# Kernel tuning notes

Measured on AMD Instinct MI355X. Metric: run time of the kernel, lower is better.

## Reference

```python
import jax, jax.numpy as jnp
import numpy as np

D_MODEL = 512
D_STATE = 64
N_LAYERS = 6
L_SEQ = 784
BATCH = 64


def _layernorm(x, g, b, eps=1e-5):
    mu = x.mean(-1, keepdims=True)
    var = ((x - mu) ** 2).mean(-1, keepdims=True)
    return (x - mu) * jax.lax.rsqrt(var + eps) * g + b


def _s4d_kernel(log_dt, log_A_real, A_imag, C_re, C_im, L):
    # log_dt: (H,), others: (H, N). Returns real conv kernel (H, L).
    dt = jnp.exp(log_dt)[:, None]                      # (H,1)
    A = -jnp.exp(log_A_real) + 1j * A_imag             # (H,N) complex
    C = C_re + 1j * C_im                               # (H,N)
    dtA = A * dt                                       # (H,N)
    Cd = C * (jnp.exp(dtA) - 1.0) / A                  # ZOH-discretized C
    # Vandermonde: V[h,n,l] = exp(dtA[h,n] * l)
    V = jnp.exp(dtA[:, :, None] * jnp.arange(L, dtype=jnp.float32))  # (H,N,L)
    K = 2.0 * jnp.einsum('hn,hnl->hl', Cd, V).real     # (H,L)
    return K


def _s4_fftconv(u, K, D):
    # u: (B,L,H), K: (H,L), D: (H,)
    L = u.shape[1]
    uf = jnp.fft.rfft(u, 2 * L, axis=1)                # (B, L+1, H)
    kf = jnp.fft.rfft(K.T, 2 * L, axis=0)              # (L+1, H)
    y = jnp.fft.irfft(uf * kf[None], 2 * L, axis=1)[:, :L]
    return y + u * D


def setup_inputs() -> dict:
    key = jax.random.key(0)
    ks = jax.random.split(key, 12)
    H, N, NL = D_MODEL, D_STATE, N_LAYERS
    x = jax.random.normal(ks[0], (BATCH, L_SEQ, 1), dtype=jnp.float32)
    enc_w = jax.random.normal(ks[1], (1, H), dtype=jnp.float32) * 0.5
    enc_b = jnp.zeros((H,), dtype=jnp.float32)
    # S4D-Lin style init, stacked over layers
    log_dt = jnp.tile(
        jax.random.uniform(ks[2], (H,), minval=np.log(0.001), maxval=np.log(0.1)),
        (NL, 1))                                        # (NL,H)
    log_A_real = jnp.full((NL, H, N), jnp.log(0.5), dtype=jnp.float32)
    A_imag = jnp.tile(np.pi * jnp.arange(N, dtype=jnp.float32), (NL, H, 1))
    C_re = jax.random.normal(ks[3], (NL, H, N), dtype=jnp.float32) * (0.5 ** 0.5)
    C_im = jax.random.normal(ks[4], (NL, H, N), dtype=jnp.float32) * (0.5 ** 0.5)
    D = jax.random.normal(ks[5], (NL, H), dtype=jnp.float32)
    ln_g = jnp.ones((NL, H), dtype=jnp.float32)
    ln_b = jnp.zeros((NL, H), dtype=jnp.float32)
    fn_g = jnp.ones((H,), dtype=jnp.float32)
    fn_b = jnp.zeros((H,), dtype=jnp.float32)
    dec_w = jax.random.normal(ks[6], (H, 10), dtype=jnp.float32) / jnp.sqrt(H)
    dec_b = jnp.zeros((10,), dtype=jnp.float32)
    return dict(x=x, enc_w=enc_w, enc_b=enc_b, log_dt=log_dt,
                log_A_real=log_A_real, A_imag=A_imag, C_re=C_re, C_im=C_im,
                D=D, ln_g=ln_g, ln_b=ln_b, fn_g=fn_g, fn_b=fn_b,
                dec_w=dec_w, dec_b=dec_b)


def reference(x, enc_w, enc_b, log_dt, log_A_real, A_imag, C_re, C_im, D,
              ln_g, ln_b, fn_g, fn_b, dec_w, dec_b):
    h = x @ enc_w + enc_b                               # (B,L,H)
    L = h.shape[1]
    for i in range(log_dt.shape[0]):                    # fixed n_layers
        K = _s4d_kernel(log_dt[i], log_A_real[i], A_imag[i], C_re[i], C_im[i], L)
        z = _s4_fftconv(h, K, D[i])                     # S4 output (dropout=eval)
        h = _layernorm(h + z, ln_g[i], ln_b[i])         # residual + LN
    h = _layernorm(h, fn_g, fn_b)
    h = h.mean(axis=1)                                  # mean pool over seq
    return h @ dec_w + dec_b                            # (B,10)
```

## Files before the change

### kernel.cpp

```cpp
#include <hip/hip_runtime.h>
#include <hip/hip_bf16.h>

#define HD 512
#define NST 64
#define NLAY 6
#define LSEQ 784
#define BB 64
#define NKA 848
#define TOFF 800
#define LPADROWS 800
#define KSTR 850
#define CHK2 5
#define NCH 5
#define UTS2 9

typedef unsigned short u16;
typedef short s8v __attribute__((ext_vector_type(8)));
typedef float f16v __attribute__((ext_vector_type(16)));
typedef u16  u4h __attribute__((ext_vector_type(4)));
typedef u16  u8h __attribute__((ext_vector_type(8)));

__device__ __forceinline__ unsigned f2b(float f)
{
    unsigned u = __builtin_bit_cast(unsigned, f);
    return (u + 0x7FFFu + ((u >> 16) & 1u)) >> 16;
}
__device__ __forceinline__ float b2f16(u16 v)
{
    unsigned u = ((unsigned)v) << 16;
    return __builtin_bit_cast(float, u);
}
__device__ __forceinline__ unsigned pkbf(float lo, float hi)
{
    unsigned r;
    asm("v_cvt_pk_bf16_f32 %0, %1, %2" : "=v"(r) : "v"(lo), "v"(hi));
    return r;
}

__global__ void precompute_k(const float* __restrict__ log_dt,
                             const float* __restrict__ log_A_real,
                             const float* __restrict__ A_imag,
                             const float* __restrict__ C_re,
                             const float* __restrict__ C_im,
                             float* __restrict__ lamr, float* __restrict__ lami,
                             float* __restrict__ dtr,  float* __restrict__ dti,
                             float* __restrict__ c2r,  float* __restrict__ c2i)
{
    int t = blockIdx.x * 256 + threadIdx.x;
    if (t >= NLAY * HD * NST) return;
    int ih = t >> 6;
    float dt  = expf(log_dt[ih]);
    float are = -expf(log_A_real[t]);
    float aim = A_imag[t];
    float dr = are * dt, di = aim * dt;
    float er = expf(dr);
    float sn, cs; __sincosf(di, &sn, &cs);
    float lr = er * cs, li = er * sn;
    float e1r = lr - 1.0f, e1i = li;
    float den = are * are + aim * aim;
    float qr = (e1r * are + e1i * aim) / den;
    float qi = (e1i * are - e1r * aim) / den;
    float crv = C_re[t], civ = C_im[t];
    lamr[t] = lr; lami[t] = li; dtr[t] = dr; dti[t] = di;
    c2r[t] = 2.0f * (crv * qr - civ * qi);
    c2i[t] = 2.0f * (crv * qi + civ * qr);
}

__global__ void kq_k(const float* __restrict__ lamr, const float* __restrict__ lami,
                     const float* __restrict__ dtr,  const float* __restrict__ dti,
                     const float* __restrict__ c2r,  const float* __restrict__ c2i,
                     u16* __restrict__ KA)
{
    int t = blockIdx.x * 256 + threadIdx.x;
    int dc = t % 49;
    int ih = t / 49;
    int d0 = dc * 16;
    float acc[16];
#pragma unroll
    for (int k = 0; k < 16; k++) acc[k] = 0.f;
    int base = ih * 64;
    for (int n = 0; n < 64; n++) {
        float lr = lamr[base + n], li = lami[base + n];
        float dr = dtr[base + n],  di = dti[base + n];
        float cr = c2r[base + n],  ci = c2i[base + n];
        float e = __expf(dr * (float)d0);
        float sn, cs; __sincosf(di * (float)d0, &sn, &cs);
        float pr = e * cs, pi = e * sn;
#pragma unroll
        for (int k = 0; k < 16; k++) {
            acc[k] = fmaf(cr, pr, fmaf(-ci, pi, acc[k]));
            float nr = pr * lr - pi * li;
            pi = fmaf(pr, li, pi * lr);
            pr = nr;
        }
    }
    u16* kap = KA + (size_t)ih * NKA;
#pragma unroll
    for (int k = 0; k < 16; k++)
        kap[TOFF - (d0 + k)] = (u16)f2b(acc[k]);
    if (dc == 0)  for (int z = TOFF + 1; z < NKA; z++) kap[z] = 0;
    if (dc == 48) for (int z = 0; z < TOFF - 783; z++) kap[z] = 0;
}

__global__ void xt_k(const float* __restrict__ x, float* __restrict__ xT)
{
    int t = blockIdx.x * 256 + threadIdx.x;
    int l = t >> 6, b = t & 63;
    xT[t] = x[b * LSEQ + l];
}

__global__ void encoder_k(const float* __restrict__ xT, const float* __restrict__ ew,
                          const float* __restrict__ eb, u16* __restrict__ Vb)
{
    int g = blockIdx.x * 256 + threadIdx.x;
    int bo = g & 7;
    int h  = (g >> 3) & 511;
    int l  = g >> 12;
    const float4* xp = (const float4*)&xT[l * BB + 8 * bo];
    float4 a0 = xp[0], a1 = xp[1];
    float w = ew[h], bb = eb[h];
    unsigned p0 = f2b(fmaf(a0.x, w, bb)) | (f2b(fmaf(a0.y, w, bb)) << 16);
    unsigned p1 = f2b(fmaf(a0.z, w, bb)) | (f2b(fmaf(a0.w, w, bb)) << 16);
    unsigned p2 = f2b(fmaf(a1.x, w, bb)) | (f2b(fmaf(a1.y, w, bb)) << 16);
    unsigned p3 = f2b(fmaf(a1.z, w, bb)) | (f2b(fmaf(a1.w, w, bb)) << 16);
    *(uint4*)&Vb[((size_t)l * HD + h) * BB + 8 * bo] = (uint4){p0, p1, p2, p3};
}

__global__ __launch_bounds__(256)
void stats_k(const u16* __restrict__ P, float2* __restrict__ M)
{
    __shared__ float redS[32][65], redQ[32][65];
    const int thr = threadIdx.x;
    const size_t l = blockIdx.x;
    if (l >= LSEQ) {
        if (thr < BB) M[l * BB + thr] = make_float2(0.f, 1.f);
        return;
    }
    const int bo = thr & 7;
    const int ho = thr >> 3;
    const u16* sp = &P[(l * HD + (size_t)ho * 16) * BB + 8 * bo];
    float s[8] = {0, 0, 0, 0, 0, 0, 0, 0};
    float q[8] = {0, 0, 0, 0, 0, 0, 0, 0};
#pragma unroll
    for (int k = 0; k < 16; k++) {
        u8h r = *(const u8h*)(sp + (size_t)k * BB);
#pragma unroll
        for (int i = 0; i < 8; i++) {
            float x = b2f16(r[i]);
            s[i] += x;
            q[i] = fmaf(x, x, q[i]);
        }
    }
#pragma unroll
    for (int i = 0; i < 8; i++) { redS[ho][8 * bo + i] = s[i]; redQ[ho][8 * bo + i] = q[i]; }
    __syncthreads();
    if (thr < 64) {
        float ts = 0.f, tq = 0.f;
#pragma unroll
        for (int g = 0; g < 32; g++) { ts += redS[g][thr]; tq += redQ[g][thr]; }
        float mu = ts * (1.0f / HD);
        float rs = rsqrtf(tq * (1.0f / HD) - mu * mu + 1e-5f);
        M[l * BB + thr] = make_float2(mu, rs);
    }
}

template<int FLN>
__global__ __launch_bounds__(128, 4)
void conv_k(const u16* __restrict__ Vb, u16* __restrict__ V2,
            const u16* __restrict__ KA, const float* __restrict__ Dvec,
            const float2* __restrict__ M,
            const float* __restrict__ gp, const float* __restrict__ bp)
{
    __shared__ __align__(16) u16 KR[6816];
    __shared__ __align__(16) unsigned UT[2][64 * UTS2];

    const int thr = threadIdx.x;
    const int bid = blockIdx.x;
    const int c   = NCH - 1 - (bid >> 9);
    const int h   = bid & 511;
    const int w   = thr >> 6;
    const int lane = thr & 63;
    const int n2 = lane & 31;
    const int qp = lane >> 5;
    const int JTN = 10 * c + 10;

    const float gh = FLN ? gp[h] : 0.f;
    const float bh = FLN ? bp[h] : 0.f;

    const u16* kap = KA + (size_t)h * NKA;
    {
        int s = thr & 7, ch = thr >> 3;
        int i0 = ch * 53;
        int i1 = (i0 + 53 < NKA) ? (i0 + 53) : NKA;
        u16* kr = KR + KSTR * s + ((8 - s) & 7);
        for (int i = i0; i < i1; i++) kr[i] = kap[i];
    }

    const int jj = thr >> 4;
    const int bq = thr & 15;
    {
        const int j = 2 * jj;
        const u16* p = &Vb[((size_t)j * HD + h) * BB + 4 * bq];
        u4h r0 = *(const u4h*)p;
        u4h r1 = *(const u4h*)(p + (size_t)HD * BB);
        unsigned* up = &UT[0][0];
        if (FLN) {
            const float4* m0p = (const float4*)&M[(size_t)j * BB + 4 * bq];
            const float4* m1p = (const float4*)&M[(size_t)(j + 1) * BB + 4 * bq];
            float4 a0 = m0p[0], a1 = m0p[1], b0 = m1p[0], b1 = m1p[1];
            float A0[4] = {a0.y * gh, a0.w * gh, a1.y * gh, a1.w * gh};
            float C0[4] = {fmaf(-a0.x, A0[0], bh), fmaf(-a0.z, A0[1], bh),
                           fmaf(-a1.x, A0[2], bh), fmaf(-a1.z, A0[3], bh)};
            float A1[4] = {b0.y * gh, b0.w * gh, b1.y * gh, b1.w * gh};
            float C1[4] = {fmaf(-b0.x, A1[0], bh), fmaf(-b0.z, A1[1], bh),
                           fmaf(-b1.x, A1[2], bh), fmaf(-b1.z, A1[3], bh)};
#pragma unroll
            for (int i = 0; i < 4; i++) {
                float x0 = fmaf(b2f16(r0[i]), A0[i], C0[i]);
                float x1 = fmaf(b2f16(r1[i]), A1[i], C1[i]);
                up[(4 * bq + i) * UTS2 + jj] = pkbf(x0, x1);
            }
        } else {
#pragma unroll
            for (int i = 0; i < 4; i++)
                up[(4 * bq + i) * UTS2 + jj] = (unsigned)r0[i] | ((unsigned)r1[i] << 16);
        }
    }
    __syncthreads();

    f16v acc[CHK2];
#pragma unroll
    for (int i = 0; i < CHK2; i++)
#pragma unroll
        for (int r = 0; r < 16; r++) acc[i][r] = 0.f;

    const float dcoef = 1.0f + Dvec[h];

    const int s = lane & 7;
    const u16* krb = KR + KSTR * s + ((8 - s) & 7)
                     + (TOFF - 160 * c) + 8 * qp - n2;
    const unsigned* bb0 = &UT[0][(32 * w + n2) * UTS2 + 4 * qp];
    const unsigned* bb1 = &UT[1][(32 * w + n2) * UTS2 + 4 * qp];

    for (int jt = 0; jt < JTN; ++jt) {
        u4h r0, r1;
        float4 mA0, mB0, mA1, mB1;
        const bool more = (jt + 1) < JTN;
        if (more) {
            int j = 16 * (jt + 1) + 2 * jj;
            const u16* p = &Vb[((size_t)j * HD + h) * BB + 4 * bq];
            r0 = *(const u4h*)p;
            r1 = *(const u4h*)(p + (size_t)HD * BB);
            if (FLN) {
                const float4* m0p = (const float4*)&M[(size_t)j * BB + 4 * bq];
                const float4* m1p = (const float4*)&M[(size_t)(j + 1) * BB + 4 * bq];
                mA0 = m0p[0]; mB0 = m0p[1]; mA1 = m1p[0]; mB1 = m1p[1];
            }
        }
        const unsigned* bb = (jt & 1) ? bb1 : bb0;
        union { unsigned u[4]; s8v v; } bu;
        bu.u[0] = bb[0]; bu.u[1] = bb[1]; bu.u[2] = bb[2]; bu.u[3] = bb[3];

        const u16* ap0 = krb + 16 * jt;
#pragma unroll
        for (int lt = 0; lt < CHK2; ++lt) {
            if (jt > 10 * c + 2 * lt + 1) continue;
            s8v av = *(const s8v*)__builtin_assume_aligned(ap0 - 32 * lt, 16);
            acc[lt] = __builtin_amdgcn_mfma_f32_32x32x16_bf16(av, bu.v, acc[lt], 0, 0, 0);
        }
        if (more) {
            unsigned* up = &UT[(jt & 1) ^ 1][0];
            if (FLN) {
                float A0[4] = {mA0.y * gh, mA0.w * gh, mB0.y * gh, mB0.w * gh};
                float C0[4] = {fmaf(-mA0.x, A0[0], bh), fmaf(-mA0.z, A0[1], bh),
                               fmaf(-mB0.x, A0[2], bh), fmaf(-mB0.z, A0[3], bh)};
                float A1[4] = {mA1.y * gh, mA1.w * gh, mB1.y * gh, mB1.w * gh};
                float C1[4] = {fmaf(-mA1.x, A1[0], bh), fmaf(-mA1.z, A1[1], bh),
                               fmaf(-mB1.x, A1[2], bh), fmaf(-mB1.z, A1[3], bh)};
#pragma unroll
                for (int i = 0; i < 4; i++) {
                    float x0 = fmaf(b2f16(r0[i]), A0[i], C0[i]);
                    float x1 = fmaf(b2f16(r1[i]), A1[i], C1[i]);
                    up[(4 * bq + i) * UTS2 + jj] = pkbf(x0, x1);
                }
            } else {
#pragma unroll
                for (int i = 0; i < 4; i++)
                    up[(4 * bq + i) * UTS2 + jj] = (unsigned)r0[i] | ((unsigned)r1[i] << 16);
            }
        }
        __syncthreads();
    }

#pragma unroll
    for (int lt = 0; lt < CHK2; ++lt) {
        const int l0 = 32 * (5 * c + lt) + 4 * qp;
#pragma unroll
        for (int r = 0; r < 16; ++r) {
            int l = l0 + (r & 3) + 8 * (r >> 2);
            size_t a = ((size_t)l * HD + h) * BB + 32 * w + n2;
            float x = b2f16(Vb[a]);
            float u = x;
            if (FLN) {
                float2 m = M[(size_t)l * BB + 32 * w + n2];
                u = fmaf(x - m.x, m.y * gh, bh);
            }
            V2[a] = (u16)f2b(fmaf(dcoef, u, acc[lt][r]));
        }
    }
}

__global__ __launch_bounds__(512)
void lnT2_k(const u16* __restrict__ src, u16* __restrict__ dst,
            const float2* __restrict__ M,
            const float* __restrict__ g5p, const float* __restrict__ b5p,
            const float* __restrict__ gp, const float* __restrict__ bp)
{
    __shared__ float redS[64][65], redQ[64][65];
    __shared__ float mus[64], rss[64];
    __shared__ float gs[512], bs[512];
    const int thr = threadIdx.x;
    const int bo = thr & 7;
    const int hg = thr >> 3;
    const size_t l = blockIdx.x;
    gs[thr] = gp[thr]; bs[thr] = bp[thr];

    const float4* mp = (const float4*)&M[l * BB + 8 * bo];
    float4 m0 = mp[0], m1 = mp[1], m2 = mp[2], m3 = mp[3];
    float mu5[8] = {m0.x, m0.z, m1.x, m1.z, m2.x, m2.z, m3.x, m3.z};
    float rs5[8] = {m0.y, m0.w, m1.y, m1.w, m2.y, m2.w, m3.y, m3.w};

    const u16* sp = &src[(l * HD + (size_t)hg * 8) * BB + 8 * bo];
    float v[64];
    float s[8] = {0, 0, 0, 0, 0, 0, 0, 0};
    float q[8] = {0, 0, 0, 0, 0, 0, 0, 0};
#pragma unroll
    for (int k = 0; k < 8; k++) {
        u8h r = *(const u8h*)(sp + (size_t)k * BB);
        float g5 = g5p[hg * 8 + k], b5 = b5p[hg * 8 + k];
#pragma unroll
        for (int i = 0; i < 8; i++) {
            float x = fmaf(b2f16(r[i]) - mu5[i], rs5[i] * g5, b5);
            v[k * 8 + i] = x;
            s[i] += x;
            q[i] = fmaf(x, x, q[i]);
        }
    }
#pragma unroll
    for (int i = 0; i < 8; i++) { redS[hg][8 * bo + i] = s[i]; redQ[hg][8 * bo + i] = q[i]; }
    __syncthreads();
    if (thr < 64) {
        float ts = 0.f, tq = 0.f;
#pragma unroll
        for (int g = 0; g < 64; g++) { ts += redS[g][thr]; tq += redQ[g][thr]; }
        float mu = ts * (1.0f / HD);
        mus[thr] = mu;
        rss[thr] = rsqrtf(tq * (1.0f / HD) - mu * mu + 1e-5f);
    }
    __syncthreads();
    float mu[8], rs[8];
#pragma unroll
    for (int i = 0; i < 8; i++) { mu[i] = mus[8 * bo + i]; rs[i] = rss[8 * bo + i]; }
    u16* dp = &dst[(l * HD + (size_t)hg * 8) * BB + 8 * bo];
#pragma unroll
    for (int k = 0; k < 8; k++) {
        float g = gs[hg * 8 + k], bb = bs[hg * 8 + k];
        u8h wv;
#pragma unroll
        for (int i = 0; i < 8; i++)
            wv[i] = (u16)f2b(fmaf((v[k * 8 + i] - mu[i]) * rs[i], g, bb));
        *(u8h*)(dp + (size_t)k * BB) = wv;
    }
}

__global__ void pool_k(const u16* __restrict__ Vb, float* __restrict__ PO)
{
    __shared__ float red[4][64];
    int h = blockIdx.x;
    int b = threadIdx.x & 63;
    int lg = threadIdx.x >> 6;
    const u16* p = &Vb[(size_t)h * BB + b];
    float s = 0.f;
    for (int l = lg; l < LSEQ; l += 4) s += b2f16(p[(size_t)l * HD * BB]);
    red[lg][b] = s;
    __syncthreads();
    if (threadIdx.x < 64) {
        float t = red[0][b] + red[1][b] + red[2][b] + red[3][b];
        PO[h * BB + b] = t * (1.0f / LSEQ);
    }
}

__global__ void dec_k(const float* __restrict__ PO, const float* __restrict__ w,
                      const float* __restrict__ bias, float* __restrict__ out)
{
    int t = blockIdx.x * 256 + threadIdx.x;
    if (t >= BB * 10) return;
    int cc = t % 10, b = t / 10;
    float acc = bias[cc];
    for (int hh = 0; hh < HD; hh++)
        acc = fmaf(PO[hh * BB + b], w[hh * 10 + cc], acc);
    out[t] = acc;
}

extern "C" void kernel_launch(void* const* d_in, const int* in_sizes, int n_in,
                              void* d_out, int out_size, void* d_ws, size_t ws_size,
                              hipStream_t stream)
{
    const float* x   = (const float*)d_in[0];
    const float* ew  = (const float*)d_in[1];
    const float* eb  = (const float*)d_in[2];
    const float* ldt = (const float*)d_in[3];
    const float* lar = (const float*)d_in[4];
    const float* aim = (const float*)d_in[5];
    const float* cre = (const float*)d_in[6];
    const float* cim = (const float*)d_in[7];
    const float* Dp  = (const float*)d_in[8];
    const float* lng = (const float*)d_in[9];
    const float* lnb = (const float*)d_in[10];
    const float* fng = (const float*)d_in[11];
    const float* fnb = (const float*)d_in[12];
    const float* dw  = (const float*)d_in[13];
    const float* db  = (const float*)d_in[14];
    float* out = (float*)d_out;

    const size_t SZB = (size_t)BB * LPADROWS * HD;
    const size_t PP  = (size_t)NLAY * HD * NST;
    u16*   Vb  = (u16*)d_ws;
    u16*   V2  = Vb + SZB;
    float* PAR = (float*)(V2 + SZB);
    float* lamr = PAR,        * lami = PAR + PP;
    float* dtr  = PAR + 2*PP, * dti  = PAR + 3*PP;
    float* c2r  = PAR + 4*PP, * c2i  = PAR + 5*PP;
    u16* KA = (u16*)(PAR + 6 * PP);
    float* PO = PAR + 6 * PP + (NLAY * HD * NKA) / 2;
    float* xT = PO + BB * HD;
    float2* M = (float2*)PAR;

    precompute_k<<<(NLAY * HD * NST + 255) / 256, 256, 0, stream>>>(
        ldt, lar, aim, cre, cim, lamr, lami, dtr, dti, c2r, c2i);
    kq_k<<<(NLAY * HD * 49) / 256, 256, 0, stream>>>(
        lamr, lami, dtr, dti, c2r, c2i, KA);
    xt_k<<<(LSEQ * BB) / 256, 256, 0, stream>>>(x, xT);
    encoder_k<<<(LSEQ * HD * 8) / 256, 256, 0, stream>>>(xT, ew, eb, Vb);

    conv_k<0><<<512 * NCH, 128, 0, stream>>>(Vb, V2, KA, Dp, M, lng, lnb);
    stats_k<<<LPADROWS, 256, 0, stream>>>(V2, M);
    for (int i = 1; i < NLAY; i++) {
        const u16* srcb = (i & 1) ? V2 : Vb;
        u16*       dstb = (i & 1) ? Vb : V2;
        conv_k<1><<<512 * NCH, 128, 0, stream>>>(
            srcb, dstb, KA + (size_t)i * HD * NKA, Dp + i * HD,
            M, lng + (size_t)(i - 1) * HD, lnb + (size_t)(i - 1) * HD);
        stats_k<<<LPADROWS, 256, 0, stream>>>(dstb, M);
    }
    lnT2_k<<<LSEQ, 512, 0, stream>>>(Vb, Vb, M, lng + 5 * HD, lnb + 5 * HD, fng, fnb);
    pool_k<<<HD, 256, 0, stream>>>(Vb, PO);
    dec_k<<<(BB * 10 + 255) / 256, 256, 0, stream>>>(PO, dw, db, out);
}
```

Before: 656.5 us.

## Restructure causal conv to keep Toeplitz kernel fragments in registers per channel

Replaces the chunked conv kernel (512x5 blocks, kernel row staged in LDS) with one block per channel. Each block preloads all 25x2 Toeplitz A-fragments into registers from a dual-shifted kernel layout, so every fragment load is aligned. The block then stages the whole padded input sequence into a large swizzled LDS buffer in five groups and reuses it for the residual/D term in the epilogue. The intent is to drop the per-chunk kernel reloads and the redundant input re-reads across chunks. In exchange it launches only 512 blocks with heavy register pressure (launch_bounds 128,1) and large LDS, which hurts occupancy and latency hiding.

```diff
diff --git a/kernel.cpp b/kernel.cpp
--- a/kernel.cpp
+++ b/kernel.cpp
@@ -6,18 +6,13 @@
 #define NLAY 6
 #define LSEQ 784
 #define BB 64
-#define NKA 848
 #define TOFF 800
 #define LPADROWS 800
-#define KSTR 850
-#define CHK2 5
-#define NCH 5
-#define UTS2 9
+#define KROW 850
 
 typedef unsigned short u16;
 typedef short s8v __attribute__((ext_vector_type(8)));
 typedef float f16v __attribute__((ext_vector_type(16)));
-typedef u16  u4h __attribute__((ext_vector_type(4)));
 typedef u16  u8h __attribute__((ext_vector_type(8)));
 
 __device__ __forceinline__ unsigned f2b(float f)
@@ -69,7 +64,7 @@
 __global__ void kq_k(const float* __restrict__ lamr, const float* __restrict__ lami,
                      const float* __restrict__ dtr,  const float* __restrict__ dti,
                      const float* __restrict__ c2r,  const float* __restrict__ c2i,
-                     u16* __restrict__ KA)
+                     u16* __restrict__ KAS)
 {
     int t = blockIdx.x * 256 + threadIdx.x;
     int dc = t % 49;
@@ -94,12 +89,23 @@
             pr = nr;
         }
     }
-    u16* kap = KA + (size_t)ih * NKA;
-#pragma unroll
-    for (int k = 0; k < 16; k++)
-        kap[TOFF - (d0 + k)] = (u16)f2b(acc[k]);
-    if (dc == 0)  for (int z = TOFF + 1; z < NKA; z++) kap[z] = 0;
-    if (dc == 48) for (int z = 0; z < TOFF - 783; z++) kap[z] = 0;
+    u16* r0p = KAS + (size_t)ih * 2 * KROW;
+    u16* r1p = r0p + KROW;
+#pragma unroll
+    for (int k = 0; k < 16; k++) {
+        u16 vb = (u16)f2b(acc[k]);
+        int tt = TOFF - (d0 + k);
+        r0p[tt] = vb;
+        r1p[1 + tt] = vb;
+    }
+    if (dc == 0) {
+        for (int z = TOFF + 1; z < KROW; z++) r0p[z] = 0;
+        for (int z = TOFF + 2; z < KROW; z++) r1p[z] = 0;
+        r1p[0] = 0;
+    }
+    if (dc == 48) {
+        for (int z = 0; z < TOFF - 783; z++) { r0p[z] = 0; r1p[1 + z] = 0; }
+    }
 }
 
 __global__ void xt_k(const float* __restrict__ x, float* __restrict__ xT)
@@ -116,6 +122,8 @@
     int bo = g & 7;
     int h  = (g >> 3) & 511;
     int l  = g >> 12;
+    uint4* dst = (uint4*)&Vb[((size_t)l * HD + h) * BB + 8 * bo];
+    if (l >= LSEQ) { *dst = (uint4){0, 0, 0, 0}; return; }
     const float4* xp = (const float4*)&xT[l * BB + 8 * bo];
     float4 a0 = xp[0], a1 = xp[1];
     float w = ew[h], bb = eb[h];
@@ -123,7 +131,7 @@
     unsigned p1 = f2b(fmaf(a0.z, w, bb)) | (f2b(fmaf(a0.w, w, bb)) << 16);
     unsigned p2 = f2b(fmaf(a1.x, w, bb)) | (f2b(fmaf(a1.y, w, bb)) << 16);
     unsigned p3 = f2b(fmaf(a1.z, w, bb)) | (f2b(fmaf(a1.w, w, bb)) << 16);
-    *(uint4*)&Vb[((size_t)l * HD + h) * BB + 8 * bo] = (uint4){p0, p1, p2, p3};
+    *dst = (uint4){p0, p1, p2, p3};
 }
 
 __global__ __launch_bounds__(256)
@@ -165,148 +173,140 @@
 }
 
 template<int FLN>
-__global__ __launch_bounds__(128, 4)
-void conv_k(const u16* __restrict__ Vb, u16* __restrict__ V2,
-            const u16* __restrict__ KA, const float* __restrict__ Dvec,
-            const float2* __restrict__ M,
-            const float* __restrict__ gp, const float* __restrict__ bp)
-{
-    __shared__ __align__(16) u16 KR[6816];
-    __shared__ __align__(16) unsigned UT[2][64 * UTS2];
+__global__ __launch_bounds__(128, 1)
+void sconv_k(const u16* __restrict__ Vb, u16* __restrict__ V2,
+             const u16* __restrict__ KAS, const float* __restrict__ Dvec,
+             const float2* __restrict__ M,
+             const float* __restrict__ gp, const float* __restrict__ bp)
+{
+    __shared__ __align__(16) unsigned SB[25 * 64 * 20];
 
     const int thr = threadIdx.x;
-    const int bid = blockIdx.x;
-    const int c   = NCH - 1 - (bid >> 9);
-    const int h   = bid & 511;
+    const int h   = blockIdx.x;
+    const int lane = thr & 63;
     const int w   = thr >> 6;
-    const int lane = thr & 63;
-    const int n2 = lane & 31;
-    const int qp = lane >> 5;
-    const int JTN = 10 * c + 10;
+    const int n2  = lane & 31;
+    const int qp  = lane >> 5;
 
     const float gh = FLN ? gp[h] : 0.f;
     const float bh = FLN ? bp[h] : 0.f;
-
-    const u16* kap = KA + (size_t)h * NKA;
+    const float dcoef = 1.0f + Dvec[h];
+
+    s8v afr[25][2];
     {
-        int s = thr & 7, ch = thr >> 3;
-        int i0 = ch * 53;
-        int i1 = (i0 + 53 < NKA) ? (i0 + 53) : NKA;
-        u16* kr = KR + KSTR * s + ((8 - s) & 7);
-        for (int i = i0; i < i1; i++) kr[i] = kap[i];
-    }
-
-    const int jj = thr >> 4;
-    const int bq = thr & 15;
-    {
-        const int j = 2 * jj;
-        const u16* p = &Vb[((size_t)j * HD + h) * BB + 4 * bq];
-        u4h r0 = *(const u4h*)p;
-        u4h r1 = *(const u4h*)(p + (size_t)HD * BB);
-        unsigned* up = &UT[0][0];
-        if (FLN) {
-            const float4* m0p = (const float4*)&M[(size_t)j * BB + 4 * bq];
-            const float4* m1p = (const float4*)&M[(size_t)(j + 1) * BB + 4 * bq];
-            float4 a0 = m0p[0], a1 = m0p[1], b0 = m1p[0], b1 = m1p[1];
-            float A0[4] = {a0.y * gh, a0.w * gh, a1.y * gh, a1.w * gh};
-            float C0[4] = {fmaf(-a0.x, A0[0], bh), fmaf(-a0.z, A0[1], bh),
-                           fmaf(-a1.x, A0[2], bh), fmaf(-a1.z, A0[3], bh)};
-            float A1[4] = {b0.y * gh, b0.w * gh, b1.y * gh, b1.w * gh};
-            float C1[4] = {fmaf(-b0.x, A1[0], bh), fmaf(-b0.z, A1[1], bh),
-                           fmaf(-b1.x, A1[2], bh), fmaf(-b1.z, A1[3], bh)};
-#pragma unroll
-            for (int i = 0; i < 4; i++) {
-                float x0 = fmaf(b2f16(r0[i]), A0[i], C0[i]);
-                float x1 = fmaf(b2f16(r1[i]), A1[i], C1[i]);
-                up[(4 * bq + i) * UTS2 + jj] = pkbf(x0, x1);
+        const int sA = n2 & 1;
+        const u16* kb = KAS + ((size_t)h * 2 + sA) * KROW + sA
+                        + TOFF - n2 + 8 * qp;
+#pragma unroll
+        for (int dd = 0; dd < 25; dd++)
+#pragma unroll
+            for (int ch = 0; ch < 2; ch++) {
+                const u16* kp = kb - 32 * dd + 16 * ch;
+                union { unsigned uu[4]; s8v v; } af;
+#pragma unroll
+                for (int q = 0; q < 4; q++)
+                    af.uu[q] = *(const unsigned*)(kp + 2 * q);
+                afr[dd][ch] = af.v;
             }
-        } else {
-#pragma unroll
-            for (int i = 0; i < 4; i++)
-                up[(4 * bq + i) * UTS2 + jj] = (unsigned)r0[i] | ((unsigned)r1[i] << 16);
-        }
-    }
-    __syncthreads();
-
-    f16v acc[CHK2];
-#pragma unroll
-    for (int i = 0; i < CHK2; i++)
-#pragma unroll
-        for (int r = 0; r < 16; r++) acc[i][r] = 0.f;
-
-    const float dcoef = 1.0f + Dvec[h];
-
-    const int s = lane & 7;
-    const u16* krb = KR + KSTR * s + ((8 - s) & 7)
-                     + (TOFF - 160 * c) + 8 * qp - n2;
-    const unsigned* bb0 = &UT[0][(32 * w + n2) * UTS2 + 4 * qp];
-    const unsigned* bb1 = &UT[1][(32 * w + n2) * UTS2 + 4 * qp];
-
-    for (int jt = 0; jt < JTN; ++jt) {
-        u4h r0, r1;
-        float4 mA0, mB0, mA1, mB1;
-        const bool more = (jt + 1) < JTN;
-        if (more) {
-            int j = 16 * (jt + 1) + 2 * jj;
-            const u16* p = &Vb[((size_t)j * HD + h) * BB + 4 * bq];
-            r0 = *(const u4h*)p;
-            r1 = *(const u4h*)(p + (size_t)HD * BB);
+    }
+
+    auto STAGE = [&](int g0) {
+#pragma unroll
+        for (int j5 = 0; j5 < 5; j5++) {
+            int u  = thr + 128 * j5;
+            int rp = u >> 3;
+            int sg = u & 7;
+            int r0 = 160 * g0 + 2 * rp;
+            const u16* p = &Vb[((size_t)r0 * HD + h) * BB + 8 * sg];
+            u8h ra = *(const u8h*)p;
+            u8h rb = *(const u8h*)(p + (size_t)HD * BB);
+            unsigned ov[8];
             if (FLN) {
-                const float4* m0p = (const float4*)&M[(size_t)j * BB + 4 * bq];
-                const float4* m1p = (const float4*)&M[(size_t)(j + 1) * BB + 4 * bq];
-                mA0 = m0p[0]; mB0 = m0p[1]; mA1 = m1p[0]; mB1 = m1p[1];
-            }
-        }
-        const unsigned* bb = (jt & 1) ? bb1 : bb0;
-        union { unsigned u[4]; s8v v; } bu;
-        bu.u[0] = bb[0]; bu.u[1] = bb[1]; bu.u[2] = bb[2]; bu.u[3] = bb[3];
-
-        const u16* ap0 = krb + 16 * jt;
-#pragma unroll
-        for (int lt = 0; lt < CHK2; ++lt) {
-            if (jt > 10 * c + 2 * lt + 1) continue;
-            s8v av = *(const s8v*)__builtin_assume_aligned(ap0 - 32 * lt, 16);
-            acc[lt] = __builtin_amdgcn_mfma_f32_32x32x16_bf16(av, bu.v, acc[lt], 0, 0, 0);
-        }
-        if (more) {
-            unsigned* up = &UT[(jt & 1) ^ 1][0];
-            if (FLN) {
-                float A0[4] = {mA0.y * gh, mA0.w * gh, mB0.y * gh, mB0.w * gh};
-                float C0[4] = {fmaf(-mA0.x, A0[0], bh), fmaf(-mA0.z, A0[1], bh),
-                               fmaf(-mB0.x, A0[2], bh), fmaf(-mB0.z, A0[3], bh)};
-                float A1[4] = {mA1.y * gh, mA1.w * gh, mB1.y * gh, mB1.w * gh};
-                float C1[4] = {fmaf(-mA1.x, A1[0], bh), fmaf(-mA1.z, A1[1], bh),
-                               fmaf(-mB1.x, A1[2], bh), fmaf(-mB1.z, A1[3], bh)};
+                const float4* m0 = (const float4*)&M[(size_t)r0 * BB + 8 * sg];
+                const float4* m1 = (const float4*)&M[(size_t)(r0 + 1) * BB + 8 * sg];
 #pragma unroll
                 for (int i = 0; i < 4; i++) {
-                    float x0 = fmaf(b2f16(r0[i]), A0[i], C0[i]);
-                    float x1 = fmaf(b2f16(r1[i]), A1[i], C1[i]);
-                    up[(4 * bq + i) * UTS2 + jj] = pkbf(x0, x1);
+                    float4 ma = m0[i], mb = m1[i];
+                    float A0 = ma.y * gh, C0 = fmaf(-ma.x, A0, bh);
+                    float A1 = ma.w * gh, C1 = fmaf(-ma.z, A1, bh);
+                    float B0 = mb.y * gh, D0 = fmaf(-mb.x, B0, bh);
+                    float B1 = mb.w * gh, D1 = fmaf(-mb.z, B1, bh);
+                    float x0 = fmaf(b2f16(ra[2 * i]),     A0, C0);
+                    float x1 = fmaf(b2f16(ra[2 * i + 1]), A1, C1);
+                    float y0 = fmaf(b2f16(rb[2 * i]),     B0, D0);
+                    float y1 = fmaf(b2f16(rb[2 * i + 1]), B1, D1);
+                    ov[2 * i]     = pkbf(x0, y0);
+                    ov[2 * i + 1] = pkbf(x1, y1);
                 }
             } else {
 #pragma unroll
-                for (int i = 0; i < 4; i++)
-                    up[(4 * bq + i) * UTS2 + jj] = (unsigned)r0[i] | ((unsigned)r1[i] << 16);
+                for (int i = 0; i < 8; i++)
+                    ov[i] = (unsigned)ra[i] | ((unsigned)rb[i] << 16);
             }
-        }
+            int tt = 5 * g0 + (rp >> 4);
+            int jj = rp & 15;
+            unsigned* dst = &SB[(tt * 64 + 8 * sg) * 20 + (jj ^ ((sg & 3) << 2))];
+#pragma unroll
+            for (int k = 0; k < 8; k++) dst[k * 20] = ov[k];
+        }
+    };
+
+    const int bcol = 32 * w + n2;
+    const int swz  = ((bcol >> 3) & 3) << 2;
+    const unsigned* bb0 = &SB[bcol * 20 + ((4 * qp) ^ swz)];
+    const unsigned* bb1 = &SB[bcol * 20 + ((8 + 4 * qp) ^ swz)];
+
+    STAGE(0);
+    __syncthreads();
+
+#pragma unroll
+    for (int g = 0; g < 5; g++) {
+        f16v acc[5];
+#pragma unroll
+        for (int i = 0; i < 5; i++)
+#pragma unroll
+            for (int r = 0; r < 16; r++) acc[i][r] = 0.f;
+
+#pragma unroll
+        for (int t = 0; t < 25; t++) {
+            if (t <= 5 * g + 4) {
+                s8v bv0 = *(const s8v*)__builtin_assume_aligned(bb0 + t * 1280, 16);
+                s8v bv1 = *(const s8v*)__builtin_assume_aligned(bb1 + t * 1280, 16);
+#pragma unroll
+                for (int Ti = 0; Ti < 5; Ti++) {
+                    if (5 * g + Ti >= t) {
+                        acc[Ti] = __builtin_amdgcn_mfma_f32_32x32x16_bf16(
+                            afr[5 * g + Ti - t][0], bv0, acc[Ti], 0, 0, 0);
+                        acc[Ti] = __builtin_amdgcn_mfma_f32_32x32x16_bf16(
+                            afr[5 * g + Ti - t][1], bv1, acc[Ti], 0, 0, 0);
+                    }
+                }
+            }
+        }
+
+#pragma unroll
+        for (int Ti = 0; Ti < 5; Ti++) {
+            const int T = 5 * g + Ti;
+#pragma unroll
+            for (int k = 0; k < 4; k++) {
+                int jjE = (2 * qp + 4 * k) ^ swz;
+                const uint2 dw = *(const uint2*)__builtin_assume_aligned(
+                    &SB[(T * 64 + bcol) * 20 + jjE], 8);
+                float u0 = b2f16((u16)(dw.x & 0xffff));
+                float u1 = b2f16((u16)(dw.x >> 16));
+                float u2 = b2f16((u16)(dw.y & 0xffff));
+                float u3 = b2f16((u16)(dw.y >> 16));
+                int l = 32 * T + 8 * k + 4 * qp;
+                size_t a = ((size_t)l * HD + h) * BB + bcol;
+                V2[a]                       = (u16)f2b(fmaf(dcoef, u0, acc[Ti][4 * k + 0]));
+                V2[a + (size_t)HD * BB]     = (u16)f2b(fmaf(dcoef, u1, acc[Ti][4 * k + 1]));
+                V2[a + (size_t)2 * HD * BB] = (u16)f2b(fmaf(dcoef, u2, acc[Ti][4 * k + 2]));
+                V2[a + (size_t)3 * HD * BB] = (u16)f2b(fmaf(dcoef, u3, acc[Ti][4 * k + 3]));
+            }
+        }
+
+        if (g < 4) STAGE(g + 1);
         __syncthreads();
-    }
-
-#pragma unroll
-    for (int lt = 0; lt < CHK2; ++lt) {
-        const int l0 = 32 * (5 * c + lt) + 4 * qp;
-#pragma unroll
-        for (int r = 0; r < 16; ++r) {
-            int l = l0 + (r & 3) + 8 * (r >> 2);
-            size_t a = ((size_t)l * HD + h) * BB + 32 * w + n2;
-            float x = b2f16(Vb[a]);
-            float u = x;
-            if (FLN) {
-                float2 m = M[(size_t)l * BB + 32 * w + n2];
-                u = fmaf(x - m.x, m.y * gh, bh);
-            }
-            V2[a] = (u16)f2b(fmaf(dcoef, u, acc[lt][r]));
-        }
     }
 }
 
@@ -431,25 +431,25 @@
     float* lamr = PAR,        * lami = PAR + PP;
     float* dtr  = PAR + 2*PP, * dti  = PAR + 3*PP;
     float* c2r  = PAR + 4*PP, * c2i  = PAR + 5*PP;
-    u16* KA = (u16*)(PAR + 6 * PP);
-    float* PO = PAR + 6 * PP + (NLAY * HD * NKA) / 2;
+    u16* KAS = (u16*)(PAR + 6 * PP);
+    float* PO = (float*)(KAS + (size_t)NLAY * HD * 2 * KROW);
     float* xT = PO + BB * HD;
     float2* M = (float2*)PAR;
 
     precompute_k<<<(NLAY * HD * NST + 255) / 256, 256, 0, stream>>>(
         ldt, lar, aim, cre, cim, lamr, lami, dtr, dti, c2r, c2i);
     kq_k<<<(NLAY * HD * 49) / 256, 256, 0, stream>>>(
-        lamr, lami, dtr, dti, c2r, c2i, KA);
+        lamr, lami, dtr, dti, c2r, c2i, KAS);
     xt_k<<<(LSEQ * BB) / 256, 256, 0, stream>>>(x, xT);
-    encoder_k<<<(LSEQ * HD * 8) / 256, 256, 0, stream>>>(xT, ew, eb, Vb);
-
-    conv_k<0><<<512 * NCH, 128, 0, stream>>>(Vb, V2, KA, Dp, M, lng, lnb);
+    encoder_k<<<(LPADROWS * HD * 8) / 256, 256, 0, stream>>>(xT, ew, eb, Vb);
+
+    sconv_k<0><<<HD, 128, 0, stream>>>(Vb, V2, KAS, Dp, M, lng, lnb);
     stats_k<<<LPADROWS, 256, 0, stream>>>(V2, M);
     for (int i = 1; i < NLAY; i++) {
         const u16* srcb = (i & 1) ? V2 : Vb;
         u16*       dstb = (i & 1) ? Vb : V2;
-        conv_k<1><<<512 * NCH, 128, 0, stream>>>(
-            srcb, dstb, KA + (size_t)i * HD * NKA, Dp + i * HD,
+        sconv_k<1><<<HD, 128, 0, stream>>>(
+            srcb, dstb, KAS + (size_t)i * HD * 2 * KROW, Dp + i * HD,
             M, lng + (size_t)(i - 1) * HD, lnb + (size_t)(i - 1) * HD);
         stats_k<<<LPADROWS, 256, 0, stream>>>(dstb, M);
     }
```

Result: slower. 860.9 us (+31.1%).

## Prefetch conv input two tiles ahead and interleave kernel-gen state updates

Applied to the files above, without the earlier changes.

The conv kernel's global-to-LDS staging becomes a two-deep software pipeline. Loads for tile jt+2 are issued before the MFMAs of tile jt, and the LDS write for tile jt+1 happens between the B-fragment read and the MFMAs, which gives global latency more time to hide. The Vandermonde kernel-generation loop now processes four states at once, exposing independent FMA chains for more ILP. The encoder also zero-fills the padded rows up to LPADROWS, because the deeper prefetch now reads those rows and must see defined data.

```diff
diff --git a/kernel.cpp b/kernel.cpp
--- a/kernel.cpp
+++ b/kernel.cpp
@@ -79,19 +79,27 @@
 #pragma unroll
     for (int k = 0; k < 16; k++) acc[k] = 0.f;
     int base = ih * 64;
-    for (int n = 0; n < 64; n++) {
-        float lr = lamr[base + n], li = lami[base + n];
-        float dr = dtr[base + n],  di = dti[base + n];
-        float cr = c2r[base + n],  ci = c2i[base + n];
-        float e = __expf(dr * (float)d0);
-        float sn, cs; __sincosf(di * (float)d0, &sn, &cs);
-        float pr = e * cs, pi = e * sn;
+    for (int n = 0; n < 64; n += 4) {
+        float lr[4], li[4], cr[4], ci[4], pr[4], pi[4];
+#pragma unroll
+        for (int j = 0; j < 4; j++) {
+            int q = base + n + j;
+            lr[j] = lamr[q]; li[j] = lami[q];
+            float dr = dtr[q], di = dti[q];
+            cr[j] = c2r[q]; ci[j] = c2i[q];
+            float e = __expf(dr * (float)d0);
+            float sn, cs; __sincosf(di * (float)d0, &sn, &cs);
+            pr[j] = e * cs; pi[j] = e * sn;
+        }
 #pragma unroll
         for (int k = 0; k < 16; k++) {
-            acc[k] = fmaf(cr, pr, fmaf(-ci, pi, acc[k]));
-            float nr = pr * lr - pi * li;
-            pi = fmaf(pr, li, pi * lr);
-            pr = nr;
+#pragma unroll
+            for (int j = 0; j < 4; j++) {
+                acc[k] = fmaf(cr[j], pr[j], fmaf(-ci[j], pi[j], acc[k]));
+                float nr = pr[j] * lr[j] - pi[j] * li[j];
+                pi[j] = fmaf(pr[j], li[j], pi[j] * lr[j]);
+                pr[j] = nr;
+            }
         }
     }
     u16* kap = KA + (size_t)ih * NKA;
@@ -116,6 +124,8 @@
     int bo = g & 7;
     int h  = (g >> 3) & 511;
     int l  = g >> 12;
+    uint4* dst = (uint4*)&Vb[((size_t)l * HD + h) * BB + 8 * bo];
+    if (l >= LSEQ) { *dst = (uint4){0, 0, 0, 0}; return; }
     const float4* xp = (const float4*)&xT[l * BB + 8 * bo];
     float4 a0 = xp[0], a1 = xp[1];
     float w = ew[h], bb = eb[h];
@@ -123,7 +133,7 @@
     unsigned p1 = f2b(fmaf(a0.z, w, bb)) | (f2b(fmaf(a0.w, w, bb)) << 16);
     unsigned p2 = f2b(fmaf(a1.x, w, bb)) | (f2b(fmaf(a1.y, w, bb)) << 16);
     unsigned p3 = f2b(fmaf(a1.z, w, bb)) | (f2b(fmaf(a1.w, w, bb)) << 16);
-    *(uint4*)&Vb[((size_t)l * HD + h) * BB + 8 * bo] = (uint4){p0, p1, p2, p3};
+    *dst = (uint4){p0, p1, p2, p3};
 }
 
 __global__ __launch_bounds__(256)
@@ -198,22 +208,29 @@
 
     const int jj = thr >> 4;
     const int bq = thr & 15;
-    {
-        const int j = 2 * jj;
+
+    auto LOADT = [&](int jt, u4h& r0, u4h& r1,
+                     float4& mA0, float4& mB0, float4& mA1, float4& mB1) {
+        int j = 16 * jt + 2 * jj;
         const u16* p = &Vb[((size_t)j * HD + h) * BB + 4 * bq];
-        u4h r0 = *(const u4h*)p;
-        u4h r1 = *(const u4h*)(p + (size_t)HD * BB);
-        unsigned* up = &UT[0][0];
+        r0 = *(const u4h*)p;
+        r1 = *(const u4h*)(p + (size_t)HD * BB);
         if (FLN) {
             const float4* m0p = (const float4*)&M[(size_t)j * BB + 4 * bq];
             const float4* m1p = (const float4*)&M[(size_t)(j + 1) * BB + 4 * bq];
-            float4 a0 = m0p[0], a1 = m0p[1], b0 = m1p[0], b1 = m1p[1];
-            float A0[4] = {a0.y * gh, a0.w * gh, a1.y * gh, a1.w * gh};
-            float C0[4] = {fmaf(-a0.x, A0[0], bh), fmaf(-a0.z, A0[1], bh),
-                           fmaf(-a1.x, A0[2], bh), fmaf(-a1.z, A0[3], bh)};
-            float A1[4] = {b0.y * gh, b0.w * gh, b1.y * gh, b1.w * gh};
-            float C1[4] = {fmaf(-b0.x, A1[0], bh), fmaf(-b0.z, A1[1], bh),
-                           fmaf(-b1.x, A1[2], bh), fmaf(-b1.z, A1[3], bh)};
+            mA0 = m0p[0]; mB0 = m0p[1]; mA1 = m1p[0]; mB1 = m1p[1];
+        }
+    };
+    auto WRITET = [&](int jt, u4h r0, u4h r1,
+                      float4 mA0, float4 mB0, float4 mA1, float4 mB1) {
+        unsigned* up = &UT[jt & 1][0];
+        if (FLN) {
+            float A0[4] = {mA0.y * gh, mA0.w * gh, mB0.y * gh, mB0.w * gh};
+            float C0[4] = {fmaf(-mA0.x, A0[0], bh), fmaf(-mA0.z, A0[1], bh),
+                           fmaf(-mB0.x, A0[2], bh), fmaf(-mB0.z, A0[3], bh)};
+            float A1[4] = {mA1.y * gh, mA1.w * gh, mB1.y * gh, mB1.w * gh};
+            float C1[4] = {fmaf(-mA1.x, A1[0], bh), fmaf(-mA1.z, A1[1], bh),
+                           fmaf(-mB1.x, A1[2], bh), fmaf(-mB1.z, A1[3], bh)};
 #pragma unroll
             for (int i = 0; i < 4; i++) {
                 float x0 = fmaf(b2f16(r0[i]), A0[i], C0[i]);
@@ -225,7 +242,15 @@
             for (int i = 0; i < 4; i++)
                 up[(4 * bq + i) * UTS2 + jj] = (unsigned)r0[i] | ((unsigned)r1[i] << 16);
         }
-    }
+    };
+
+    {
+        u4h t0, t1; float4 a0, a1, a2, a3;
+        LOADT(0, t0, t1, a0, a1, a2, a3);
+        WRITET(0, t0, t1, a0, a1, a2, a3);
+    }
+    u4h cr0, cr1; float4 cm0, cm1, cm2, cm3;
+    LOADT(1, cr0, cr1, cm0, cm1, cm2, cm3);
     __syncthreads();
 
     f16v acc[CHK2];
@@ -242,24 +267,15 @@
     const unsigned* bb0 = &UT[0][(32 * w + n2) * UTS2 + 4 * qp];
     const unsigned* bb1 = &UT[1][(32 * w + n2) * UTS2 + 4 * qp];
 
+    u4h nr0, nr1; float4 nm0, nm1, nm2, nm3;
     for (int jt = 0; jt < JTN; ++jt) {
-        u4h r0, r1;
-        float4 mA0, mB0, mA1, mB1;
-        const bool more = (jt + 1) < JTN;
-        if (more) {
-            int j = 16 * (jt + 1) + 2 * jj;
-            const u16* p = &Vb[((size_t)j * HD + h) * BB + 4 * bq];
-            r0 = *(const u4h*)p;
-            r1 = *(const u4h*)(p + (size_t)HD * BB);
-            if (FLN) {
-                const float4* m0p = (const float4*)&M[(size_t)j * BB + 4 * bq];
-                const float4* m1p = (const float4*)&M[(size_t)(j + 1) * BB + 4 * bq];
-                mA0 = m0p[0]; mB0 = m0p[1]; mA1 = m1p[0]; mB1 = m1p[1];
-            }
-        }
+        if (jt + 2 < JTN) LOADT(jt + 2, nr0, nr1, nm0, nm1, nm2, nm3);
+
         const unsigned* bb = (jt & 1) ? bb1 : bb0;
         union { unsigned u[4]; s8v v; } bu;
         bu.u[0] = bb[0]; bu.u[1] = bb[1]; bu.u[2] = bb[2]; bu.u[3] = bb[3];
+
+        if (jt + 1 < JTN) WRITET(jt + 1, cr0, cr1, cm0, cm1, cm2, cm3);
 
         const u16* ap0 = krb + 16 * jt;
 #pragma unroll
@@ -268,27 +284,8 @@
             s8v av = *(const s8v*)__builtin_assume_aligned(ap0 - 32 * lt, 16);
             acc[lt] = __builtin_amdgcn_mfma_f32_32x32x16_bf16(av, bu.v, acc[lt], 0, 0, 0);
         }
-        if (more) {
-            unsigned* up = &UT[(jt & 1) ^ 1][0];
-            if (FLN) {
-                float A0[4] = {mA0.y * gh, mA0.w * gh, mB0.y * gh, mB0.w * gh};
-                float C0[4] = {fmaf(-mA0.x, A0[0], bh), fmaf(-mA0.z, A0[1], bh),
-                               fmaf(-mB0.x, A0[2], bh), fmaf(-mB0.z, A0[3], bh)};
-                float A1[4] = {mA1.y * gh, mA1.w * gh, mB1.y * gh, mB1.w * gh};
-                float C1[4] = {fmaf(-mA1.x, A1[0], bh), fmaf(-mA1.z, A1[1], bh),
-                               fmaf(-mB1.x, A1[2], bh), fmaf(-mB1.z, A1[3], bh)};
-#pragma unroll
-                for (int i = 0; i < 4; i++) {
-                    float x0 = fmaf(b2f16(r0[i]), A0[i], C0[i]);
-                    float x1 = fmaf(b2f16(r1[i]), A1[i], C1[i]);
-                    up[(4 * bq + i) * UTS2 + jj] = pkbf(x0, x1);
-                }
-            } else {
-#pragma unroll
-                for (int i = 0; i < 4; i++)
-                    up[(4 * bq + i) * UTS2 + jj] = (unsigned)r0[i] | ((unsigned)r1[i] << 16);
-            }
-        }
+        cr0 = nr0; cr1 = nr1;
+        cm0 = nm0; cm1 = nm1; cm2 = nm2; cm3 = nm3;
         __syncthreads();
     }
 
@@ -441,7 +438,7 @@
     kq_k<<<(NLAY * HD * 49) / 256, 256, 0, stream>>>(
         lamr, lami, dtr, dti, c2r, c2i, KA);
     xt_k<<<(LSEQ * BB) / 256, 256, 0, stream>>>(x, xT);
-    encoder_k<<<(LSEQ * HD * 8) / 256, 256, 0, stream>>>(xT, ew, eb, Vb);
+    encoder_k<<<(LPADROWS * HD * 8) / 256, 256, 0, stream>>>(xT, ew, eb, Vb);
 
     conv_k<0><<<512 * NCH, 128, 0, stream>>>(Vb, V2, KA, Dp, M, lng, lnb);
     stats_k<<<LPADROWS, 256, 0, stream>>>(V2, M);
```

Result: slower. 825.3 us (+25.7%).
